# Optimization experiments

Hardware: AMD Instinct MI355X
Metric: run time of the kernel (lower is better)

The kernel has to match this reference:

```python
import jax, jax.numpy as jnp
import numpy as np

B, S, H, E, ID, OD, RD = 128, 256, 512, 128, 30000, 64, 32
IN = H + E + 1 + OD  # rnn_input_dim: weighted + embedded + rate + online feats


def setup_inputs() -> dict:
    key = jax.random.key(0)
    ks = jax.random.split(key, 18)
    sc = 0.02
    inp = {}
    inp['input_id'] = jax.random.randint(ks[0], (B, 1), 0, ID, dtype=jnp.int32)
    inp['input_rate'] = jax.random.uniform(ks[1], (B, 1), jnp.float32)
    inp['hidden'] = jax.random.normal(ks[2], (1, B, H), jnp.float32) * 0.1
    inp['encoder_outputs'] = jax.random.normal(ks[3], (S, B, H), jnp.float32) * 0.1
    inp['attn_mask'] = (jax.random.uniform(ks[4], (B, S)) > 0.3).astype(jnp.int32).at[:, 0].set(1)
    inp['constraint_vec'] = (jax.random.uniform(ks[5], (B, ID)) > 0.5).astype(jnp.float32).at[:, 0].set(1.0)
    inp['online_features'] = jax.random.normal(ks[6], (B, OD), jnp.float32) * 0.1
    inp['rid_features'] = jax.random.normal(ks[7], (B, RD), jnp.float32) * 0.1
    inp['emb'] = jax.random.normal(ks[8], (ID, E), jnp.float32) * sc
    inp['attn_W'] = jax.random.normal(ks[9], (2 * H, H), jnp.float32) * sc
    inp['attn_b'] = jnp.zeros((H,), jnp.float32)
    inp['v_W'] = jax.random.normal(ks[10], (H,), jnp.float32) * sc
    inp['W_ih'] = jax.random.normal(ks[11], (3 * H, IN), jnp.float32) * sc
    inp['b_ih'] = jnp.zeros((3 * H,), jnp.float32)
    inp['W_hh'] = jax.random.normal(ks[12], (3 * H, H), jnp.float32) * sc
    inp['b_hh'] = jnp.zeros((3 * H,), jnp.float32)
    inp['fc_id_W'] = jax.random.normal(ks[13], (ID, H), jnp.float32) * sc
    inp['fc_id_b'] = jnp.zeros((ID,), jnp.float32)
    inp['tan_W'] = jax.random.normal(ks[14], (H, E + H), jnp.float32) * sc
    inp['tan_b'] = jnp.zeros((H,), jnp.float32)
    inp['rate_W'] = jax.random.normal(ks[15], (1, H + RD), jnp.float32) * sc
    inp['rate_b'] = jnp.zeros((1,), jnp.float32)
    return inp


def reference(input_id, input_rate, hidden, encoder_outputs, attn_mask, constraint_vec,
              online_features, rid_features, emb, attn_W, attn_b, v_W, W_ih, b_ih,
              W_hh, b_hh, fc_id_W, fc_id_b, tan_W, tan_b, rate_W, rate_b):
    h = hidden[0]                                    # [B,H]
    embedded = emb[input_id[:, 0]]                   # [B,E] (dropout p=0 -> identity)
    # --- attention ---
    enc = jnp.transpose(encoder_outputs, (1, 0, 2))  # [B,S,H]
    hid_rep = jnp.broadcast_to(h[:, None, :], (B, S, H))
    energy = jnp.tanh(jnp.concatenate([hid_rep, enc], axis=2) @ attn_W + attn_b)  # [B,S,H]
    score = energy @ v_W                             # [B,S]
    score = jnp.where(attn_mask == 0, jnp.float32(-1e10), score)
    a = jax.nn.softmax(score, axis=1)                # [B,S]
    weighted = jnp.einsum('bs,bsh->bh', a, enc)      # [B,H]
    # --- GRU step (torch gate order r,z,n) ---
    rnn_in = jnp.concatenate([weighted, embedded, input_rate, online_features], axis=1)  # [B,IN]
    gi = rnn_in @ W_ih.T + b_ih                      # [B,3H]
    gh = h @ W_hh.T + b_hh                           # [B,3H]
    r = jax.nn.sigmoid(gi[:, :H] + gh[:, :H])
    z = jax.nn.sigmoid(gi[:, H:2 * H] + gh[:, H:2 * H])
    n = jnp.tanh(gi[:, 2 * H:] + r * gh[:, 2 * H:])
    h_new = (1.0 - z) * n + z * h                    # [B,H]
    # --- masked log softmax over id_size ---
    logits = h_new @ fc_id_W.T + fc_id_b             # [B,ID]
    maxes = jnp.max(logits, axis=1, keepdims=True)
    x_exp = jnp.exp(logits - maxes) * constraint_vec
    x_sum = jnp.sum(x_exp, axis=1, keepdims=True)
    ratio_safe = jnp.where(constraint_vec > 0, x_exp / x_sum, 1.0)
    prediction_id = jnp.where(constraint_vec > 0, jnp.log(ratio_safe), -jnp.inf)  # [B,ID]
    # --- tandem rate head ---
    max_id = jnp.argmax(prediction_id, axis=1)
    id_emb = emb[max_id]                             # [B,E]
    rate_in = jax.nn.relu(jnp.concatenate([id_emb, h_new], axis=1) @ tan_W.T + tan_b)  # [B,H]
    prediction_rate = jax.nn.sigmoid(jnp.concatenate([rate_in, rid_features], axis=1) @ rate_W.T + rate_b)  # [B,1]
    return prediction_id, prediction_rate, h_new[None]  # hidden: [1,B,H]
```

## Files before the change

### kernel.cpp

```cpp
#include <hip/hip_runtime.h>
#include <math.h>

typedef __attribute__((ext_vector_type(8))) short short8;
typedef __attribute__((ext_vector_type(4))) float f32x4;
typedef __attribute__((ext_vector_type(4))) unsigned int u32x4;

constexpr int kB  = 128;
constexpr int kS  = 256;
constexpr int kH  = 512;
constexpr int kE  = 128;
constexpr int kID = 30000;
constexpr int kOD = 64;
constexpr int kRD = 32;
constexpr int kIN = kH + kE + 1 + kOD;
constexpr int kG  = 3 * kH;
constexpr int kNC = 10;

constexpr int O_PRE  = 0;
constexpr int O_RNN  = O_PRE + kB * kH;
constexpr int O_GI   = O_RNN + kB * kIN;
constexpr int O_GH   = O_GI + kB * kG;
constexpr int O_HNEW = O_GH + kB * kG;
constexpr int O_W2F  = O_HNEW + kB * kH;
constexpr int O_AH   = O_W2F + 32 * 4096;
constexpr int O_AL   = O_AH + 8 * 4096;
constexpr int O_SM   = O_AL + 8 * 4096;
constexpr int O_SS   = O_SM + kB * kNC;
constexpr int O_SBV  = O_SS + kB * kNC;
constexpr int O_SBI  = O_SBV + kB * kNC;
constexpr int O_ENCF = O_SBI + kB * kNC;
constexpr int O_SC8  = O_GI;

constexpr float kNegSentinel = -1.0e30f;

__device__ __forceinline__ float fast_tanh(float x) {
    float e = __expf(2.f * x);
    return 1.f - 2.f / (e + 1.f);
}
__device__ __forceinline__ unsigned int f2bf(float x) {
    unsigned int u = __builtin_bit_cast(unsigned int, x);
    return (u + 0x7fffu + ((u >> 16) & 1u)) >> 16;
}
__device__ __forceinline__ float bfval(float x) {
    return __builtin_bit_cast(float, f2bf(x) << 16);
}
__device__ __forceinline__ unsigned int pack2(float a, float b) {
    return f2bf(a) | (f2bf(b) << 16);
}

__global__ __launch_bounds__(256) void k_prep(
    const float* __restrict__ enc, const float* __restrict__ attn_W,
    const float* __restrict__ attn_b, const float* __restrict__ hidden,
    float* __restrict__ ws, unsigned int* __restrict__ wsu) {
    __shared__ unsigned int SMEM[16 * 260];
    const int blk = blockIdx.x;
    const int tid = threadIdx.x;
    if (blk < 2048) {
        const int l16 = tid & 15;
        const int cb0 = ((tid >> 4) & 3) * 8 + (tid >> 6) * 32;
        const float* rowp = enc + ((size_t)blk * 16 + l16) * kH + cb0;
        unsigned int* dst = wsu + O_ENCF + (size_t)blk * 4096;
        float4 va[4], vb[4];
#pragma unroll
        for (int pass = 0; pass < 4; ++pass) {
            va[pass] = *(const float4*)(rowp + pass * 128);
            vb[pass] = *(const float4*)(rowp + pass * 128 + 4);
        }
#pragma unroll
        for (int pass = 0; pass < 4; ++pass) {
            u32x4 o = {pack2(va[pass].x, va[pass].y), pack2(va[pass].z, va[pass].w),
                       pack2(vb[pass].x, vb[pass].y), pack2(vb[pass].z, vb[pass].w)};
            *(u32x4*)(dst + (pass * 256 + tid) * 4) = o;
        }
    } else if (blk < 2080) {
        const int rbh = blk - 2048;
        const int h0 = rbh * 16;
        const int hh = tid & 15, pg = tid >> 4;
#pragma unroll
        for (int pass = 0; pass < 16; ++pass) {
            int p = pg + pass * 16;
            float a = attn_W[(kH + 2 * p) * kH + h0 + hh];
            float b = attn_W[(kH + 2 * p + 1) * kH + h0 + hh];
            SMEM[hh * 260 + p] = pack2(a, b);
        }
        __syncthreads();
        unsigned int* dst = wsu + O_W2F + (size_t)rbh * 4096;
#pragma unroll
        for (int pass = 0; pass < 4; ++pass) {
            int idx4 = pass * 256 + tid;
            int l16 = idx4 & 15, quad = (idx4 >> 4) & 3, step = idx4 >> 6;
            const unsigned int* p = &SMEM[l16 * 260 + step * 16 + quad * 4];
            u32x4 v = {p[0], p[1], p[2], p[3]};
            *(u32x4*)(dst + idx4 * 4) = v;
        }
    } else {
        float* hl = (float*)SMEM;
        int idx = blk - 2080;
        int b = idx >> 1, half = idx & 1;
        int h = half * 256 + tid;
        hl[tid]       = hidden[b * kH + tid];
        hl[tid + 256] = hidden[b * kH + tid + 256];
        __syncthreads();
        float acc0 = attn_b[h], acc1 = 0.f;
        for (int k0 = 0; k0 < kH; k0 += 16) {
            float wv[16];
#pragma unroll
            for (int j = 0; j < 16; ++j) wv[j] = attn_W[(k0 + j) * kH + h];
#pragma unroll
            for (int j = 0; j < 8; ++j) {
                acc0 += hl[k0 + j] * wv[j];
                acc1 += hl[k0 + 8 + j] * wv[8 + j];
            }
        }
        ws[O_PRE + b * kH + h] = acc0 + acc1;
    }
}

__global__ __launch_bounds__(256) void k_attn(
    const unsigned int* __restrict__ encf, const unsigned int* __restrict__ w2f,
    const float* __restrict__ vW, float* __restrict__ ws) {
    __shared__ float red[128 * 33];
    const int i = blockIdx.x;
    const int s    = (i & 7) + 8 * (i >> 6);
    const int hblk = (i >> 3) & 7;
    const int tid = threadIdx.x;
    const int w = tid >> 6, L = tid & 63;
    const int quad = L >> 4, l16 = L & 15;
    const int wm = w >> 1, wn = w & 1;
    const unsigned int* ap[4];
    const unsigned int* bp[2];
#pragma unroll
    for (int mt = 0; mt < 4; ++mt)
        ap[mt] = encf + (size_t)(s * 8 + wm * 4 + mt) * 4096 + L * 4;
#pragma unroll
    for (int nt = 0; nt < 2; ++nt)
        bp[nt] = w2f + (size_t)(hblk * 4 + wn * 2 + nt) * 4096 + L * 4;
    f32x4 acc[4][2] = {};
    u32x4 abuf[2][4], bbuf[2][2];
#pragma unroll
    for (int t = 0; t < 4; ++t) abuf[0][t] = *(const u32x4*)(ap[t]);
#pragma unroll
    for (int t = 0; t < 2; ++t) bbuf[0][t] = *(const u32x4*)(bp[t]);
#pragma unroll
    for (int step = 0; step < 16; ++step) {
        const int cur = step & 1, nxt = cur ^ 1;
        if (step < 15) {
            const int off = (step + 1) * 256;
#pragma unroll
            for (int t = 0; t < 4; ++t) abuf[nxt][t] = *(const u32x4*)(ap[t] + off);
#pragma unroll
            for (int t = 0; t < 2; ++t) bbuf[nxt][t] = *(const u32x4*)(bp[t] + off);
        }
#pragma unroll
        for (int mt = 0; mt < 4; ++mt)
#pragma unroll
            for (int nt = 0; nt < 2; ++nt)
                acc[mt][nt] = __builtin_amdgcn_mfma_f32_16x16x32_bf16(
                    __builtin_bit_cast(short8, abuf[cur][mt]),
                    __builtin_bit_cast(short8, bbuf[cur][nt]), acc[mt][nt], 0, 0, 0);
    }
#pragma unroll
    for (int mt = 0; mt < 4; ++mt)
#pragma unroll
        for (int rg = 0; rg < 4; ++rg) {
            int row = wm * 64 + mt * 16 + quad * 4 + rg;
            const float* prep = &ws[O_PRE + row * kH + hblk * 64 + wn * 32];
            const float* vp = &vW[hblk * 64 + wn * 32];
            float p = 0.f;
#pragma unroll
            for (int nt = 0; nt < 2; ++nt) {
                int hc = nt * 16 + l16;
                p += vp[hc] * fast_tanh(acc[mt][nt][rg] + prep[hc]);
            }
            red[row * 33 + wn * 16 + l16] = p;
        }
    __syncthreads();
    if (tid < 128) {
        float sum = 0.f;
#pragma unroll
        for (int c = 0; c < 32; ++c) sum += red[tid * 33 + c];
        ws[O_SC8 + hblk * (kB * kS) + tid * kS + s] = sum;
    }
}

__global__ __launch_bounds__(256) void k_soft_weight(
    const float* __restrict__ enc, const int* __restrict__ mask,
    const int* __restrict__ input_id, const float* __restrict__ input_rate,
    const float* __restrict__ online, const float* __restrict__ emb,
    float* __restrict__ ws) {
    int b = blockIdx.x, hg = blockIdx.y, tid = threadIdx.x;
    __shared__ float aa[kS];
    __shared__ float sm[256];
    __shared__ float4 red4[16 * 16];
    float v = 0.f;
#pragma unroll
    for (int h8 = 0; h8 < 8; ++h8)
        v += ws[O_SC8 + h8 * (kB * kS) + b * kS + tid];
    if (mask[b * kS + tid] == 0) v = -1e10f;
    sm[tid] = v;
    __syncthreads();
    for (int o = 128; o > 0; o >>= 1) {
        if (tid < o) sm[tid] = fmaxf(sm[tid], sm[tid + o]);
        __syncthreads();
    }
    float M = sm[0];
    __syncthreads();
    float e = __expf(v - M);
    sm[tid] = e;
    __syncthreads();
    for (int o = 128; o > 0; o >>= 1) {
        if (tid < o) sm[tid] += sm[tid + o];
        __syncthreads();
    }
    aa[tid] = e / sm[0];
    __syncthreads();
    int lane = tid & 15, sg = tid >> 4;
    int col4 = hg * 16 + lane;
    const float4* enc4 = (const float4*)enc;
    float4 acc = {0.f, 0.f, 0.f, 0.f};
    for (int s = sg; s < kS; s += 16) {
        float a = aa[s];
        float4 e4 = enc4[(s * kB + b) * (kH / 4) + col4];
        acc.x += a * e4.x; acc.y += a * e4.y; acc.z += a * e4.z; acc.w += a * e4.w;
    }
    red4[sg * 16 + lane] = acc;
    __syncthreads();
    if (sg == 0) {
        float4 o = {0.f, 0.f, 0.f, 0.f};
#pragma unroll
        for (int j = 0; j < 16; ++j) {
            float4 r = red4[j * 16 + lane];
            o.x += r.x; o.y += r.y; o.z += r.z; o.w += r.w;
        }
        float* dst = &ws[O_RNN + b * kIN + col4 * 4];
        dst[0] = o.x; dst[1] = o.y; dst[2] = o.z; dst[3] = o.w;
    }
    if (hg == 0)
        for (int idx = tid; idx < kE + 1 + kOD; idx += 256) {
            int pos = kH + idx;
            float vv;
            if (idx < kE)       vv = emb[input_id[b] * kE + idx];
            else if (idx == kE) vv = input_rate[b];
            else                vv = online[b * kOD + (idx - kE - 1)];
            ws[O_RNN + b * kIN + pos] = vv;
        }
}

__global__ __launch_bounds__(256, 2) void k_gates(
    const float* __restrict__ rnn, const float* __restrict__ W_ih,
    const float* __restrict__ hid, const float* __restrict__ W_hh,
    float* __restrict__ ws) {
    __shared__ float As[16][132];
    __shared__ float Bs[16][132];
    const float* A;  const float* Bm;  float* C;
    int K, kChunk;
    if (blockIdx.y == 0) { A = rnn; Bm = W_ih; C = ws + O_GI; K = kIN; kChunk = 96; }
    else                 { A = hid; Bm = W_hh; C = ws + O_GH; K = kH;  kChunk = 64; }
    const int n0 = blockIdx.x * 128;
    const int k0 = blockIdx.z * kChunk;
    const int k1 = min(K, k0 + kChunk);
    const int tid = threadIdx.x;
    const int ri = tid >> 4, ci = tid & 15;
    const int sr = tid >> 1, sc = tid & 1;
    const int nrow = n0 + sr;
    float acc[8][8] = {};
    for (int kt = k0; kt < k1; kt += 16) {
        int kbase = kt + sc * 8;
        if (kt + 16 <= k1) {
            const float* ap = &A[sr * K + kbase];
            float4 a0 = *(const float4*)ap;
            float4 a1 = *(const float4*)(ap + 4);
            As[sc * 8 + 0][sr] = a0.x; As[sc * 8 + 1][sr] = a0.y;
            As[sc * 8 + 2][sr] = a0.z; As[sc * 8 + 3][sr] = a0.w;
            As[sc * 8 + 4][sr] = a1.x; As[sc * 8 + 5][sr] = a1.y;
            As[sc * 8 + 6][sr] = a1.z; As[sc * 8 + 7][sr] = a1.w;
            const float* bp = &Bm[(long)nrow * K + kbase];
            float4 b0 = *(const float4*)bp;
            float4 b1 = *(const float4*)(bp + 4);
            Bs[sc * 8 + 0][sr] = b0.x; Bs[sc * 8 + 1][sr] = b0.y;
            Bs[sc * 8 + 2][sr] = b0.z; Bs[sc * 8 + 3][sr] = b0.w;
            Bs[sc * 8 + 4][sr] = b1.x; Bs[sc * 8 + 5][sr] = b1.y;
            Bs[sc * 8 + 6][sr] = b1.z; Bs[sc * 8 + 7][sr] = b1.w;
        } else {
#pragma unroll
            for (int jj = 0; jj < 8; ++jj) {
                int k = kbase + jj;
                As[sc * 8 + jj][sr] = (k < k1) ? A[sr * K + k] : 0.f;
                Bs[sc * 8 + jj][sr] = (k < k1) ? Bm[(long)nrow * K + k] : 0.f;
            }
        }
        __syncthreads();
#pragma unroll
        for (int kk = 0; kk < 16; ++kk) {
            float a[8], b[8];
            *(float4*)&a[0] = *(const float4*)&As[kk][ri * 4];
            *(float4*)&a[4] = *(const float4*)&As[kk][64 + ri * 4];
            *(float4*)&b[0] = *(const float4*)&Bs[kk][ci * 4];
            *(float4*)&b[4] = *(const float4*)&Bs[kk][64 + ci * 4];
#pragma unroll
            for (int rr = 0; rr < 8; ++rr)
#pragma unroll
                for (int cc = 0; cc < 8; ++cc) acc[rr][cc] += a[rr] * b[cc];
        }
        __syncthreads();
    }
#pragma unroll
    for (int rh = 0; rh < 2; ++rh)
#pragma unroll
        for (int ii = 0; ii < 4; ++ii) {
            int m = rh * 64 + ri * 4 + ii;
#pragma unroll
            for (int ch = 0; ch < 2; ++ch)
#pragma unroll
                for (int jj = 0; jj < 4; ++jj) {
                    int n = n0 + ch * 64 + ci * 4 + jj;
                    atomicAdd(&C[m * kG + n], acc[rh * 4 + ii][ch * 4 + jj]);
                }
        }
}

__global__ __launch_bounds__(256) void k_gru(const float* __restrict__ hidden,
                                             const float* __restrict__ b_ih,
                                             const float* __restrict__ b_hh,
                                             float* __restrict__ ws,
                                             unsigned int* __restrict__ wsu,
                                             float* __restrict__ outh) {
    int idx = blockIdx.x * 256 + threadIdx.x;
    int b = idx >> 8, pair = idx & 255;
    float hn2[2];
#pragma unroll
    for (int t = 0; t < 2; ++t) {
        int j = pair * 2 + t;
        const float* gi = &ws[O_GI + b * kG];
        const float* gh = &ws[O_GH + b * kG];
        float gr = gi[j] + b_ih[j] + gh[j] + b_hh[j];
        float gz = gi[kH + j] + b_ih[kH + j] + gh[kH + j] + b_hh[kH + j];
        float r = 1.f / (1.f + expf(-gr));
        float z = 1.f / (1.f + expf(-gz));
        float n = tanhf(gi[2 * kH + j] + b_ih[2 * kH + j] +
                        r * (gh[2 * kH + j] + b_hh[2 * kH + j]));
        float hn = (1.f - z) * n + z * hidden[b * kH + j];
        ws[O_HNEW + b * kH + j] = hn;
        outh[b * kH + j] = hn;
        hn2[t] = hn;
    }
    int fidx = (b >> 4) * 4096 +
               ((pair >> 4) * 4 + ((pair >> 2) & 3)) * 64 + (b & 15) * 4 + (pair & 3);
    wsu[O_AH + fidx] = pack2(hn2[0], hn2[1]);
    wsu[O_AL + fidx] = pack2(hn2[0] - bfval(hn2[0]), hn2[1] - bfval(hn2[1]));
}

__global__ __launch_bounds__(256) void k_logits(
    const unsigned int* __restrict__ wsu, const float* __restrict__ Wm,
    const float* __restrict__ bias, float* __restrict__ C) {
    __shared__ unsigned int BH[3][64 * 18];
    __shared__ unsigned int BL[3][64 * 18];
    const unsigned int* Ahp = wsu + O_AH;
    const unsigned int* Alp = wsu + O_AL;
    const int n0 = blockIdx.x * 64;
    const int tid = threadIdx.x;
    const int w = tid >> 6, L = tid & 63;
    const int quad = L >> 4, l16 = L & 15;
    const int r = tid >> 2, seg = tid & 3;
    const int nrow = n0 + r;
    auto stage = [&](int buf, int step) {
        float bv[8] = {};
        if (nrow < kID) {
            const float* bp = &Wm[(long)nrow * kH + step * 32 + seg * 8];
            *(float4*)&bv[0] = *(const float4*)(bp);
            *(float4*)&bv[4] = *(const float4*)(bp + 4);
        }
        unsigned int* dh = &BH[buf][r * 18 + seg * 4];
        unsigned int* dl = &BL[buf][r * 18 + seg * 4];
#pragma unroll
        for (int t = 0; t < 2; ++t) {
            float x0 = bv[4 * t], x1 = bv[4 * t + 1], x2 = bv[4 * t + 2], x3 = bv[4 * t + 3];
            dh[2 * t]     = pack2(x0, x1);
            dh[2 * t + 1] = pack2(x2, x3);
            dl[2 * t]     = pack2(x0 - bfval(x0), x1 - bfval(x1));
            dl[2 * t + 1] = pack2(x2 - bfval(x2), x3 - bfval(x3));
        }
    };
    stage(0, 0);
    stage(1, 1);
    __syncthreads();
    f32x4 acc[2][4] = {};
    for (int step = 0; step < 16; ++step) {
        const int cur = step % 3;
        short8 ah[2], al[2], bh[4], bl[4];
#pragma unroll
        for (int mt = 0; mt < 2; ++mt) {
            int off = (w * 2 + mt) * 4096 + step * 256 + L * 4;
            ah[mt] = __builtin_bit_cast(short8, *(const u32x4*)(Ahp + off));
            al[mt] = __builtin_bit_cast(short8, *(const u32x4*)(Alp + off));
        }
        const unsigned int* ch = BH[cur];
        const unsigned int* cl = BL[cur];
#pragma unroll
        for (int nt = 0; nt < 4; ++nt) {
            const unsigned int* p = ch + (nt * 16 + l16) * 18 + quad * 4;
            uint2 x = *(const uint2*)p, y = *(const uint2*)(p + 2);
            u32x4 u = {x.x, x.y, y.x, y.y};
            bh[nt] = __builtin_bit_cast(short8, u);
            p = cl + (nt * 16 + l16) * 18 + quad * 4;
            x = *(const uint2*)p; y = *(const uint2*)(p + 2);
            u32x4 u2 = {x.x, x.y, y.x, y.y};
            bl[nt] = __builtin_bit_cast(short8, u2);
        }
#pragma unroll
        for (int mt = 0; mt < 2; ++mt)
#pragma unroll
            for (int nt = 0; nt < 4; ++nt) {
                acc[mt][nt] = __builtin_amdgcn_mfma_f32_16x16x32_bf16(
                    al[mt], bh[nt], acc[mt][nt], 0, 0, 0);
                acc[mt][nt] = __builtin_amdgcn_mfma_f32_16x16x32_bf16(
                    ah[mt], bl[nt], acc[mt][nt], 0, 0, 0);
                acc[mt][nt] = __builtin_amdgcn_mfma_f32_16x16x32_bf16(
                    ah[mt], bh[nt], acc[mt][nt], 0, 0, 0);
            }
        if (step + 2 < 16) stage((step + 2) % 3, step + 2);
        __syncthreads();
    }
#pragma unroll
    for (int mt = 0; mt < 2; ++mt)
#pragma unroll
        for (int rg = 0; rg < 4; ++rg) {
            int m = w * 32 + mt * 16 + quad * 4 + rg;
#pragma unroll
            for (int nt = 0; nt < 4; ++nt) {
                int n = n0 + nt * 16 + l16;
                if (n < kID) C[(long)m * kID + n] = acc[mt][nt][rg] + bias[n];
            }
        }
}

__global__ __launch_bounds__(256) void k_stats1(const float* __restrict__ logits,
                                                const float* __restrict__ cvec,
                                                float* __restrict__ ws) {
    int c = blockIdx.x, b = blockIdx.y, tid = threadIdx.x;
    constexpr int chunkE = kID / kNC;
    constexpr int chunk4 = chunkE / 4;
    const float4* lp = (const float4*)(logits + (long)b * kID + c * chunkE);
    const float4* cp = (const float4*)(cvec + (long)b * kID + c * chunkE);
    __shared__ float smm[256], sms[256], smb[256];
    __shared__ int smi[256];
    float m = -INFINITY, s = 0.f, bv = -INFINITY;
    int bi = kID;
    for (int i = tid; i < chunk4; i += 256) {
        float4 l4 = lp[i];
        float4 c4 = cp[i];
        float le[4] = {l4.x, l4.y, l4.z, l4.w};
        float ce[4] = {c4.x, c4.y, c4.z, c4.w};
#pragma unroll
        for (int jj = 0; jj < 4; ++jj) {
            float l = le[jj];
            if (l > m) { s *= __expf(m - l); m = l; }
            if (ce[jj] > 0.f) {
                s += __expf(l - m);
                if (l > bv) { bv = l; bi = c * chunkE + i * 4 + jj; }
            }
        }
    }
    smm[tid] = m; sms[tid] = s; smb[tid] = bv; smi[tid] = bi;
    __syncthreads();
    for (int o = 128; o > 0; o >>= 1) {
        if (tid < o) {
            float m1 = smm[tid], s1 = sms[tid];
            float m2 = smm[tid + o], s2 = sms[tid + o];
            float M = fmaxf(m1, m2);
            sms[tid] = s1 * __expf(m1 - M) + s2 * __expf(m2 - M);
            smm[tid] = M;
            float ov = smb[tid + o]; int oi = smi[tid + o];
            if (ov > smb[tid] || (ov == smb[tid] && oi < smi[tid])) {
                smb[tid] = ov; smi[tid] = oi;
            }
        }
        __syncthreads();
    }
    if (tid == 0) {
        ws[O_SM + b * kNC + c]  = smm[0];
        ws[O_SS + b * kNC + c]  = sms[0];
        ws[O_SBV + b * kNC + c] = smb[0];
        ((int*)ws)[O_SBI + b * kNC + c] = smi[0];
    }
}

__global__ __launch_bounds__(256) void k_finalize(const float* __restrict__ cvec,
                                                  const float* __restrict__ ws,
                                                  float* __restrict__ out) {
    int b = blockIdx.y;
    int i4 = blockIdx.x * 256 + threadIdx.x;
    if (i4 >= kID / 4) return;
    float M = -INFINITY;
#pragma unroll
    for (int c = 0; c < kNC; ++c) M = fmaxf(M, ws[O_SM + b * kNC + c]);
    float S = 0.f;
#pragma unroll
    for (int c = 0; c < kNC; ++c)
        S += ws[O_SS + b * kNC + c] * __expf(ws[O_SM + b * kNC + c] - M);
    float off = M + logf(S);
    float4* op = (float4*)(out + (long)b * kID);
    const float4* cp = (const float4*)(cvec + (long)b * kID);
    float4 l = op[i4];
    float4 c = cp[i4];
    l.x = (c.x > 0.f) ? l.x - off : kNegSentinel;
    l.y = (c.y > 0.f) ? l.y - off : kNegSentinel;
    l.z = (c.z > 0.f) ? l.z - off : kNegSentinel;
    l.w = (c.w > 0.f) ? l.w - off : kNegSentinel;
    op[i4] = l;
}

__global__ __launch_bounds__(256) void k_rate(
    const float* __restrict__ emb, const float* __restrict__ rid,
    const float* __restrict__ tanW, const float* __restrict__ tanb,
    const float* __restrict__ rateW, const float* __restrict__ rateb,
    const float* __restrict__ ws, float* __restrict__ out) {
    constexpr int KK = kE + kH;
    int b = blockIdx.x, tid = threadIdx.x;
    __shared__ float xin[KK];
    __shared__ float red[8];
    float bv = -INFINITY;
    int mid = kID;
#pragma unroll
    for (int c = 0; c < kNC; ++c) {
        float ov = ws[O_SBV + b * kNC + c];
        int oi = ((const int*)ws)[O_SBI + b * kNC + c];
        if (ov > bv || (ov == bv && oi < mid)) { bv = ov; mid = oi; }
    }
    for (int idx = tid; idx < KK; idx += 256)
        xin[idx] = (idx < kE) ? emb[mid * kE + idx] : ws[O_HNEW + b * kH + (idx - kE)];
    __syncthreads();
    int g = tid >> 5, lane = tid & 31;
    float gsum = 0.f;
    for (int jj = g; jj < kH; jj += 8) {
        const float* wr = &tanW[jj * KK];
        float acc = 0.f;
#pragma unroll
        for (int t = 0; t < KK / 32; ++t) acc += xin[lane + 32 * t] * wr[lane + 32 * t];
#pragma unroll
        for (int o = 16; o > 0; o >>= 1) acc += __shfl_down(acc, o, 32);
        if (lane == 0) gsum += fmaxf(acc + tanb[jj], 0.f) * rateW[jj];
    }
    if (lane == 0) red[g] = gsum;
    __syncthreads();
    if (tid == 0) {
        float acc = rateb[0];
#pragma unroll
        for (int gg = 0; gg < 8; ++gg) acc += red[gg];
        for (int k = 0; k < kRD; ++k) acc += rid[b * kRD + k] * rateW[kH + k];
        out[b] = 1.f / (1.f + expf(-acc));
    }
}

extern "C" void kernel_launch(void* const* d_in, const int* in_sizes, int n_in,
                              void* d_out, int out_size, void* d_ws, size_t ws_size,
                              hipStream_t stream) {
    const int*   input_id   = (const int*)  d_in[0];
    const float* input_rate = (const float*)d_in[1];
    const float* hidden     = (const float*)d_in[2];
    const float* enc        = (const float*)d_in[3];
    const int*   attn_mask  = (const int*)  d_in[4];
    const float* cvec       = (const float*)d_in[5];
    const float* online     = (const float*)d_in[6];
    const float* rid        = (const float*)d_in[7];
    const float* emb        = (const float*)d_in[8];
    const float* attn_W     = (const float*)d_in[9];
    const float* attn_b     = (const float*)d_in[10];
    const float* vW         = (const float*)d_in[11];
    const float* W_ih       = (const float*)d_in[12];
    const float* b_ih       = (const float*)d_in[13];
    const float* W_hh       = (const float*)d_in[14];
    const float* b_hh       = (const float*)d_in[15];
    const float* fc_id_W    = (const float*)d_in[16];
    const float* fc_id_b    = (const float*)d_in[17];
    const float* tan_W      = (const float*)d_in[18];
    const float* tan_b      = (const float*)d_in[19];
    const float* rate_W     = (const float*)d_in[20];
    const float* rate_b     = (const float*)d_in[21];

    float* ws         = (float*)d_ws;
    unsigned int* wsu = (unsigned int*)d_ws;
    float* out        = (float*)d_out;
    float* out_pid    = out;
    float* out_rate   = out + kB * kID;
    float* out_h      = out + kB * kID + kB;

    k_prep<<<2336, 256, 0, stream>>>(enc, attn_W, attn_b, hidden, ws, wsu);
    k_attn<<<2048, 256, 0, stream>>>(wsu + O_ENCF, wsu + O_W2F, vW, ws);
    k_soft_weight<<<dim3(128, 8), 256, 0, stream>>>(enc, attn_mask, input_id,
                                                    input_rate, online, emb, ws);
    hipMemsetAsync(ws + O_GI, 0, (size_t)2 * kB * kG * sizeof(float), stream);
    k_gates<<<dim3(kG / 128, 2, 8), 256, 0, stream>>>(ws + O_RNN, W_ih, hidden, W_hh, ws);
    k_gru<<<128, 256, 0, stream>>>(hidden, b_ih, b_hh, ws, wsu, out_h);
    k_logits<<<dim3((kID + 63) / 64), 256, 0, stream>>>(wsu, fc_id_W, fc_id_b, out_pid);
    k_stats1<<<dim3(kNC, 128), 256, 0, stream>>>(out_pid, cvec, ws);
    k_finalize<<<dim3(30, 128), 256, 0, stream>>>(cvec, ws, out_pid);
    k_rate<<<128, 256, 0, stream>>>(emb, rid, tan_W, tan_b, rate_W, rate_b, ws, out_rate);
}
```

Measured before the change: 427.9 us.

## Replace split-K atomics with partial buffers and parallelize rate head across blocks

The gate GEMM no longer zeroes the output with a memset and accumulates split-K partials through float atomics. Each K-slice now writes its own partial buffer with vector stores, and the GRU kernel sums the eight partials. Separately, the rate head is split into a 128x8-block kernel, where each warp computes eight rows, plus a small final kernel, replacing one block per batch row. This adds workspace traffic for the partial buffers and one extra launch.

```diff
diff --git a/kernel.cpp b/kernel.cpp
--- a/kernel.cpp
+++ b/kernel.cpp
@@ -30,6 +30,9 @@
 constexpr int O_SBI  = O_SBV + kB * kNC;
 constexpr int O_ENCF = O_SBI + kB * kNC;
 constexpr int O_SC8  = O_GI;
+constexpr int O_GP   = O_ENCF;
+constexpr int O_GPH  = O_GP + 8 * kB * kG;
+constexpr int O_RP   = O_PRE;
 
 constexpr float kNegSentinel = -1.0e30f;
 
@@ -252,10 +255,11 @@
     float* __restrict__ ws) {
     __shared__ float As[16][132];
     __shared__ float Bs[16][132];
-    const float* A;  const float* Bm;  float* C;
+    const float* A;  const float* Bm;  float* Cp;
     int K, kChunk;
-    if (blockIdx.y == 0) { A = rnn; Bm = W_ih; C = ws + O_GI; K = kIN; kChunk = 96; }
-    else                 { A = hid; Bm = W_hh; C = ws + O_GH; K = kH;  kChunk = 64; }
+    if (blockIdx.y == 0) { A = rnn; Bm = W_ih; Cp = ws + O_GP;  K = kIN; kChunk = 96; }
+    else                 { A = hid; Bm = W_hh; Cp = ws + O_GPH; K = kH;  kChunk = 64; }
+    Cp += (size_t)blockIdx.z * (kB * kG);
     const int n0 = blockIdx.x * 128;
     const int k0 = blockIdx.z * kChunk;
     const int k1 = min(K, k0 + kChunk);
@@ -310,12 +314,11 @@
         for (int ii = 0; ii < 4; ++ii) {
             int m = rh * 64 + ri * 4 + ii;
 #pragma unroll
-            for (int ch = 0; ch < 2; ++ch)
-#pragma unroll
-                for (int jj = 0; jj < 4; ++jj) {
-                    int n = n0 + ch * 64 + ci * 4 + jj;
-                    atomicAdd(&C[m * kG + n], acc[rh * 4 + ii][ch * 4 + jj]);
-                }
+            for (int ch = 0; ch < 2; ++ch) {
+                float4 v = {acc[rh * 4 + ii][ch * 4 + 0], acc[rh * 4 + ii][ch * 4 + 1],
+                            acc[rh * 4 + ii][ch * 4 + 2], acc[rh * 4 + ii][ch * 4 + 3]};
+                *(float4*)&Cp[(size_t)m * kG + n0 + ch * 64 + ci * 4] = v;
+            }
         }
 }
 
@@ -327,18 +330,40 @@
                                              float* __restrict__ outh) {
     int idx = blockIdx.x * 256 + threadIdx.x;
     int b = idx >> 8, pair = idx & 255;
+    int j0 = pair * 2;
+    const float* gpi = &ws[O_GP  + (size_t)b * kG + j0];
+    const float* gph = &ws[O_GPH + (size_t)b * kG + j0];
+    float2 gir = {0.f, 0.f}, giz = {0.f, 0.f}, gin = {0.f, 0.f};
+    float2 ghr = {0.f, 0.f}, ghz = {0.f, 0.f}, ghn = {0.f, 0.f};
+#pragma unroll
+    for (int z = 0; z < 8; ++z) {
+        size_t off = (size_t)z * (kB * kG);
+        float2 a0 = *(const float2*)(gpi + off);
+        float2 a1 = *(const float2*)(gpi + off + kH);
+        float2 a2 = *(const float2*)(gpi + off + 2 * kH);
+        float2 c0 = *(const float2*)(gph + off);
+        float2 c1 = *(const float2*)(gph + off + kH);
+        float2 c2 = *(const float2*)(gph + off + 2 * kH);
+        gir.x += a0.x; gir.y += a0.y; giz.x += a1.x; giz.y += a1.y;
+        gin.x += a2.x; gin.y += a2.y;
+        ghr.x += c0.x; ghr.y += c0.y; ghz.x += c1.x; ghz.y += c1.y;
+        ghn.x += c2.x; ghn.y += c2.y;
+    }
     float hn2[2];
 #pragma unroll
     for (int t = 0; t < 2; ++t) {
-        int j = pair * 2 + t;
-        const float* gi = &ws[O_GI + b * kG];
-        const float* gh = &ws[O_GH + b * kG];
-        float gr = gi[j] + b_ih[j] + gh[j] + b_hh[j];
-        float gz = gi[kH + j] + b_ih[kH + j] + gh[kH + j] + b_hh[kH + j];
+        int j = j0 + t;
+        float gi_r = t ? gir.y : gir.x;
+        float gi_z = t ? giz.y : giz.x;
+        float gi_n = t ? gin.y : gin.x;
+        float gh_r = t ? ghr.y : ghr.x;
+        float gh_z = t ? ghz.y : ghz.x;
+        float gh_n = t ? ghn.y : ghn.x;
+        float gr = gi_r + b_ih[j] + gh_r + b_hh[j];
+        float gz = gi_z + b_ih[kH + j] + gh_z + b_hh[kH + j];
         float r = 1.f / (1.f + expf(-gr));
         float z = 1.f / (1.f + expf(-gz));
-        float n = tanhf(gi[2 * kH + j] + b_ih[2 * kH + j] +
-                        r * (gh[2 * kH + j] + b_hh[2 * kH + j]));
+        float n = tanhf(gi_n + b_ih[2 * kH + j] + r * (gh_n + b_hh[2 * kH + j]));
         float hn = (1.f - z) * n + z * hidden[b * kH + j];
         ws[O_HNEW + b * kH + j] = hn;
         outh[b * kH + j] = hn;
@@ -510,13 +535,12 @@
     op[i4] = l;
 }
 
-__global__ __launch_bounds__(256) void k_rate(
-    const float* __restrict__ emb, const float* __restrict__ rid,
-    const float* __restrict__ tanW, const float* __restrict__ tanb,
-    const float* __restrict__ rateW, const float* __restrict__ rateb,
-    const float* __restrict__ ws, float* __restrict__ out) {
+__global__ __launch_bounds__(256) void k_rate1(
+    const float* __restrict__ emb, const float* __restrict__ tanW,
+    const float* __restrict__ tanb, const float* __restrict__ rateW,
+    float* __restrict__ ws) {
     constexpr int KK = kE + kH;
-    int b = blockIdx.x, tid = threadIdx.x;
+    int b = blockIdx.x, g = blockIdx.y, tid = threadIdx.x;
     __shared__ float xin[KK];
     __shared__ float red[8];
     float bv = -INFINITY;
@@ -528,28 +552,48 @@
         if (ov > bv || (ov == bv && oi < mid)) { bv = ov; mid = oi; }
     }
     for (int idx = tid; idx < KK; idx += 256)
-        xin[idx] = (idx < kE) ? emb[mid * kE + idx] : ws[O_HNEW + b * kH + (idx - kE)];
-    __syncthreads();
-    int g = tid >> 5, lane = tid & 31;
+        xin[idx] = (idx < kE) ? emb[(size_t)mid * kE + idx]
+                              : ws[O_HNEW + b * kH + (idx - kE)];
+    __syncthreads();
+    int grp = tid >> 5, lane = tid & 31;
+    int jbase = g * 64 + grp * 8;
+    const float* wr = &tanW[(size_t)jbase * KK + lane];
+    float acc[8] = {};
+#pragma unroll
+    for (int t = 0; t < KK / 32; ++t) {
+        float xv = xin[lane + 32 * t];
+#pragma unroll
+        for (int r = 0; r < 8; ++r) acc[r] += xv * wr[r * KK + 32 * t];
+    }
     float gsum = 0.f;
-    for (int jj = g; jj < kH; jj += 8) {
-        const float* wr = &tanW[jj * KK];
-        float acc = 0.f;
-#pragma unroll
-        for (int t = 0; t < KK / 32; ++t) acc += xin[lane + 32 * t] * wr[lane + 32 * t];
-#pragma unroll
-        for (int o = 16; o > 0; o >>= 1) acc += __shfl_down(acc, o, 32);
-        if (lane == 0) gsum += fmaxf(acc + tanb[jj], 0.f) * rateW[jj];
-    }
-    if (lane == 0) red[g] = gsum;
+#pragma unroll
+    for (int r = 0; r < 8; ++r) {
+        float a = acc[r];
+#pragma unroll
+        for (int o = 16; o > 0; o >>= 1) a += __shfl_down(a, o, 32);
+        if (lane == 0) gsum += fmaxf(a + tanb[jbase + r], 0.f) * rateW[jbase + r];
+    }
+    if (lane == 0) red[grp] = gsum;
     __syncthreads();
     if (tid == 0) {
-        float acc = rateb[0];
-#pragma unroll
-        for (int gg = 0; gg < 8; ++gg) acc += red[gg];
-        for (int k = 0; k < kRD; ++k) acc += rid[b * kRD + k] * rateW[kH + k];
-        out[b] = 1.f / (1.f + expf(-acc));
-    }
+        float s = 0.f;
+#pragma unroll
+        for (int r = 0; r < 8; ++r) s += red[r];
+        ws[O_RP + b * 8 + g] = s;
+    }
+}
+
+__global__ __launch_bounds__(128) void k_rate2(
+    const float* __restrict__ rid, const float* __restrict__ rateW,
+    const float* __restrict__ rateb, const float* __restrict__ ws,
+    float* __restrict__ out) {
+    int b = threadIdx.x;
+    float acc = rateb[0];
+#pragma unroll
+    for (int g = 0; g < 8; ++g) acc += ws[O_RP + b * 8 + g];
+#pragma unroll
+    for (int k = 0; k < kRD; ++k) acc += rid[b * kRD + k] * rateW[kH + k];
+    out[b] = 1.f / (1.f + expf(-acc));
 }
 
 extern "C" void kernel_launch(void* const* d_in, const int* in_sizes, int n_in,
@@ -589,11 +633,11 @@
     k_attn<<<2048, 256, 0, stream>>>(wsu + O_ENCF, wsu + O_W2F, vW, ws);
     k_soft_weight<<<dim3(128, 8), 256, 0, stream>>>(enc, attn_mask, input_id,
                                                     input_rate, online, emb, ws);
-    hipMemsetAsync(ws + O_GI, 0, (size_t)2 * kB * kG * sizeof(float), stream);
     k_gates<<<dim3(kG / 128, 2, 8), 256, 0, stream>>>(ws + O_RNN, W_ih, hidden, W_hh, ws);
     k_gru<<<128, 256, 0, stream>>>(hidden, b_ih, b_hh, ws, wsu, out_h);
     k_logits<<<dim3((kID + 63) / 64), 256, 0, stream>>>(wsu, fc_id_W, fc_id_b, out_pid);
     k_stats1<<<dim3(kNC, 128), 256, 0, stream>>>(out_pid, cvec, ws);
     k_finalize<<<dim3(30, 128), 256, 0, stream>>>(cvec, ws, out_pid);
-    k_rate<<<128, 256, 0, stream>>>(emb, rid, tan_W, tan_b, rate_W, rate_b, ws, out_rate);
-}
+    k_rate1<<<dim3(128, 8), 256, 0, stream>>>(emb, tan_W, tan_b, rate_W, ws);
+    k_rate2<<<1, 128, 0, stream>>>(rid, rate_W, rate_b, ws, out_rate);
+}
```

After: 355.6 us. 16.9% less time.
